# Performance work log

Measured on AMD Instinct MI355X. Metric: run time of the kernel, lower is better.

The kernel has to match this reference:

```python
import jax, jax.numpy as jnp
import numpy as np

N, E, IN_C, OUT_C, HEADS = 50000, 800000, 256, 256, 4
C = OUT_C // HEADS  # per-head channels = 64
BN_EPS = 1e-5


def setup_inputs() -> dict:
    key = jax.random.key(0)
    ks = jax.random.split(key, 16)
    inp = {
        'x': jax.random.normal(ks[0], (N, IN_C), dtype=jnp.float32),
        'edge_index': jax.random.randint(ks[1], (2, E), 0, N, dtype=jnp.int64),
        'edge_attr': jax.random.uniform(ks[2], (E, 1), dtype=jnp.float32),
        'spatial_coords': jax.random.normal(ks[3], (N, 2), dtype=jnp.float32),
        # GATConv params
        'W_gat': jax.random.normal(ks[4], (IN_C, HEADS * C), dtype=jnp.float32) * 0.05,
        'att_src': jax.random.normal(ks[5], (HEADS, C), dtype=jnp.float32) * 0.05,
        'att_dst': jax.random.normal(ks[6], (HEADS, C), dtype=jnp.float32) * 0.05,
        'bias_gat': jnp.zeros((HEADS * C,), dtype=jnp.float32),
        # spatial_attention MLP (computed but unused by the original forward)
        'w1': jax.random.normal(ks[7], (1, 64), dtype=jnp.float32) * 0.05,
        'b1': jnp.zeros((64,), dtype=jnp.float32),
        'w2': jax.random.normal(ks[8], (64, HEADS), dtype=jnp.float32) * 0.05,
        'b2': jnp.zeros((HEADS,), dtype=jnp.float32),
        # feature_transform: Linear + BatchNorm1d (eval stats) + ReLU (+Dropout=identity)
        'w_ft': jax.random.normal(ks[9], (IN_C, OUT_C), dtype=jnp.float32) * 0.05,
        'b_ft': jnp.zeros((OUT_C,), dtype=jnp.float32),
        'bn_gamma': jnp.ones((OUT_C,), dtype=jnp.float32),
        'bn_beta': jnp.zeros((OUT_C,), dtype=jnp.float32),
        'bn_mean': jax.random.normal(ks[10], (OUT_C,), dtype=jnp.float32) * 0.01,
        'bn_var': jax.random.uniform(ks[11], (OUT_C,), dtype=jnp.float32, minval=0.5, maxval=1.5),
    }
    return inp


def _forward(x, edge_index, edge_attr, W_gat, att_src, att_dst, bias_gat,
             w1, b1, w2, b2, w_ft, b_ft, bn_gamma, bn_beta, bn_mean, bn_var):
    n = x.shape[0]
    # add self-loops (PyG GATConv default)
    loop = jnp.arange(n, dtype=edge_index.dtype)
    src = jnp.concatenate([edge_index[0], loop])
    dst = jnp.concatenate([edge_index[1], loop])

    # linear transform: [N, heads, C]
    h = (x @ W_gat).reshape(n, HEADS, C)
    a_src = jnp.einsum('nhc,hc->nh', h, att_src)  # [N, H]
    a_dst = jnp.einsum('nhc,hc->nh', h, att_dst)  # [N, H]

    # per-edge attention logits, LeakyReLU(0.2)
    alpha = jax.nn.leaky_relu(a_src[src] + a_dst[dst], negative_slope=0.2)  # [Etot, H]
    # segment softmax over incoming edges of each destination node
    amax = jax.ops.segment_max(alpha, dst, num_segments=n)
    alpha = jnp.exp(alpha - amax[dst])
    denom = jax.ops.segment_sum(alpha, dst, num_segments=n)
    alpha = alpha / (denom[dst] + 1e-16)

    # weighted message aggregation
    msg = h[src] * alpha[:, :, None]                        # [Etot, H, C]
    agg = jax.ops.segment_sum(msg, dst, num_segments=n)     # [N, H, C]
    gat_out = agg.reshape(n, HEADS * C) + bias_gat

    # spatial attention weights (computed but UNUSED, matching original)
    spatial_weights = jax.nn.sigmoid(jax.nn.relu(edge_attr @ w1 + b1) @ w2 + b2)
    del spatial_weights

    # feature_transform (BatchNorm in eval mode, Dropout identity)
    y = x @ w_ft + b_ft
    y = (y - bn_mean) * jax.lax.rsqrt(bn_var + BN_EPS) * bn_gamma + bn_beta
    transformed = jax.nn.relu(y)

    return gat_out + transformed


def reference(x, edge_index, edge_attr, spatial_coords, W_gat, att_src, att_dst,
              bias_gat, w1, b1, w2, b2, w_ft, b_ft, bn_gamma, bn_beta, bn_mean, bn_var):
    # spatial_coords is accepted but unused by the original module's forward
    return _forward(x, edge_index, edge_attr, W_gat, att_src, att_dst, bias_gat,
                    w1, b1, w2, b2, w_ft, b_ft, bn_gamma, bn_beta, bn_mean, bn_var)
```

## Files before the change

### kernel.cpp

```cpp
#include <hip/hip_runtime.h>
#include <math.h>

typedef __attribute__((ext_vector_type(4))) float  f32x4;
typedef __attribute__((ext_vector_type(8))) short  short8;
typedef __attribute__((ext_vector_type(8))) unsigned short usx8;

__device__ __forceinline__ unsigned short f2bf(float f) {
    union { float f; unsigned int i; } c; c.f = f;
    unsigned int x = c.i;
    unsigned int r = (x + 0x7FFFu + ((x >> 16) & 1u)) >> 16;
    return (unsigned short)r;
}

__global__ __launch_bounds__(256) void k_prep1(
    int* __restrict__ zr, int zn,
    const float* __restrict__ Wg, const float* __restrict__ Wf,
    unsigned short* __restrict__ wbt, int nz) {
    int b = blockIdx.x;
    if (b < nz) {
        int i = b * 256 + threadIdx.x;
        if (i < zn) zr[i] = 0;
        return;
    }
    b -= nz;
    int idx = b * 256 + threadIdx.x;
    int c = idx >> 8;
    int k = idx & 255;
    float v = (c < 256) ? Wg[k * 256 + c] : Wf[k * 256 + (c - 256)];
    wbt[idx] = f2bf(v);
}

__global__ __launch_bounds__(256) void k_prep2(
    const float* __restrict__ x, unsigned short* __restrict__ xb, long total8, int nx,
    const int* __restrict__ ei, int* __restrict__ deg, int E) {
    int b = blockIdx.x;
    if (b < nx) {
        long i = (long)b * 256 + threadIdx.x;
        if (i >= total8) return;
        const f32x4* p = (const f32x4*)x;
        f32x4 v0 = p[2 * i], v1 = p[2 * i + 1];
        usx8 o;
        o[0] = f2bf(v0[0]); o[1] = f2bf(v0[1]); o[2] = f2bf(v0[2]); o[3] = f2bf(v0[3]);
        o[4] = f2bf(v1[0]); o[5] = f2bf(v1[1]); o[6] = f2bf(v1[2]); o[7] = f2bf(v1[3]);
        ((usx8*)xb)[i] = o;
        return;
    }
    int i = (b - nx) * 256 + threadIdx.x;
    if (i < E) atomicAdd(&deg[ei[E + i]], 1);
}

#define BM 128
#define BN 128

__global__ __launch_bounds__(256, 4) void k_gemm_scan(
    const unsigned short* __restrict__ xb,
    const unsigned short* __restrict__ wbt,
    unsigned short* __restrict__ hb,
    unsigned short* __restrict__ tb,
    float* __restrict__ out,
    const float* __restrict__ att_s, const float* __restrict__ att_d,
    float* __restrict__ a_src, float* __restrict__ a_dst,
    const float* __restrict__ b_ft, const float* __restrict__ bn_g,
    const float* __restrict__ bn_b, const float* __restrict__ bn_m,
    const float* __restrict__ bn_v, int M, int ngemm,
    const int* __restrict__ deg, int* __restrict__ offs, int* __restrict__ bsum) {
    __shared__ unsigned short As[128 * 64];
    __shared__ unsigned short Bs[128 * 64];
    __shared__ int tmp[256];

    if (blockIdx.x >= ngemm) {
        int b = blockIdx.x - ngemm, t = threadIdx.x;
        int base = b * 1024;
        int v[4];
#pragma unroll
        for (int j = 0; j < 4; j++) {
            int i = base + t * 4 + j;
            v[j] = (i < M) ? (deg[i] + 1) : 0;
        }
        int local = v[0] + v[1] + v[2] + v[3];
        tmp[t] = local;
        __syncthreads();
        for (int off = 1; off < 256; off <<= 1) {
            int xv = (t >= off) ? tmp[t - off] : 0;
            __syncthreads();
            tmp[t] += xv;
            __syncthreads();
        }
        int run = tmp[t] - local;
        if (t == 255) bsum[b] = tmp[255];
#pragma unroll
        for (int j = 0; j < 4; j++) {
            int i = base + t * 4 + j;
            if (i < M) offs[i] = run;
            run += v[j];
        }
        return;
    }

    const int t = threadIdx.x;
    const int w = t >> 6, l = t & 63;
    const int wr = w >> 1, wc = w & 1;
    const int bm0 = (blockIdx.x >> 2) * BM;
    const int bn0 = (blockIdx.x & 3) * BN;
    const int kg = l >> 4;
    const int lm = l & 15;

    const int srow = l >> 3;
    const int scol = ((l & 7) ^ srow) << 3;

    f32x4 acc[4][4] = {};

    for (int kk = 0; kk < 4; kk++) {
        const int k0 = kk * 64;
        __syncthreads();
#pragma unroll
        for (int j = 0; j < 4; j++) {
            int r = ((w * 4 + j) << 3) + srow;
            int ga = bm0 + r; if (ga >= M) ga = M - 1;
            __builtin_amdgcn_global_load_lds(
                (const __attribute__((address_space(1))) unsigned int*)
                    (xb + (long)ga * 256 + k0 + scol),
                (__attribute__((address_space(3))) unsigned int*)
                    (As + ((w * 4 + j) << 9)),
                16, 0, 0);
            __builtin_amdgcn_global_load_lds(
                (const __attribute__((address_space(1))) unsigned int*)
                    (wbt + (long)(bn0 + r) * 256 + k0 + scol),
                (__attribute__((address_space(3))) unsigned int*)
                    (Bs + ((w * 4 + j) << 9)),
                16, 0, 0);
        }
        __syncthreads();
#pragma unroll
        for (int ks = 0; ks < 2; ks++) {
            const int cb = (ks * 64 + kg * 16) ^ ((lm & 7) << 4);
            short8 afr[4], bfr[4];
#pragma unroll
            for (int mi = 0; mi < 4; mi++) {
                int row = wr * 64 + mi * 16 + lm;
                afr[mi] = *(const short8*)((const char*)As + row * 128 + cb);
            }
#pragma unroll
            for (int nj = 0; nj < 4; nj++) {
                int row = wc * 64 + nj * 16 + lm;
                bfr[nj] = *(const short8*)((const char*)Bs + row * 128 + cb);
            }
#pragma unroll
            for (int mi = 0; mi < 4; mi++)
#pragma unroll
                for (int nj = 0; nj < 4; nj++)
                    acc[mi][nj] = __builtin_amdgcn_mfma_f32_16x16x32_bf16(
                        afr[mi], bfr[nj], acc[mi][nj], 0, 0, 0);
        }
    }

    const bool isH = (bn0 < 256);
#pragma unroll
    for (int mi = 0; mi < 4; mi++) {
#pragma unroll
        for (int nj = 0; nj < 4; nj++) {
            int col = bn0 + wc * 64 + nj * 16 + lm;
            f32x4 a = acc[mi][nj];
            int rowbase = bm0 + wr * 64 + mi * 16 + kg * 4;
            if (isH) {
#pragma unroll
                for (int r = 0; r < 4; r++) {
                    int row = rowbase + r;
                    if (row < M) hb[(long)row * 256 + col] = f2bf(a[r]);
                }
            } else {
                int c2 = col - 256;
                float bft = b_ft[c2], mu = bn_m[c2];
                float iv = rsqrtf(bn_v[c2] + 1e-5f);
                float g = bn_g[c2], bt = bn_b[c2];
#pragma unroll
                for (int r = 0; r < 4; r++) {
                    int row = rowbase + r;
                    if (row < M) {
                        float v = (a[r] + bft - mu) * iv * g + bt;
                        v = v > 0.f ? v : 0.f;
                        if (tb) tb[(long)row * 256 + c2] = f2bf(v);
                        else    out[(long)row * 256 + c2] = v;
                    }
                }
            }
        }
    }

    if (isH) {
        const int head = (bn0 >> 6) + wc;
        float as_c[4], ad_c[4];
#pragma unroll
        for (int nj = 0; nj < 4; nj++) {
            as_c[nj] = att_s[head * 64 + nj * 16 + lm];
            ad_c[nj] = att_d[head * 64 + nj * 16 + lm];
        }
#pragma unroll
        for (int mi = 0; mi < 4; mi++) {
#pragma unroll
            for (int r = 0; r < 4; r++) {
                float s1 = 0.f, s2 = 0.f;
#pragma unroll
                for (int nj = 0; nj < 4; nj++) {
                    s1 = fmaf(acc[mi][nj][r], as_c[nj], s1);
                    s2 = fmaf(acc[mi][nj][r], ad_c[nj], s2);
                }
#pragma unroll
                for (int o = 1; o < 16; o <<= 1) {
                    s1 += __shfl_xor(s1, o);
                    s2 += __shfl_xor(s2, o);
                }
                int row = bm0 + wr * 64 + mi * 16 + kg * 4 + r;
                if (lm == 0 && row < M) {
                    a_src[(long)row * 4 + head] = s1;
                    a_dst[(long)row * 4 + head] = s2;
                }
            }
        }
    }
}

#define BK 32
__global__ __launch_bounds__(256) void k_gemm(
    const float* __restrict__ x, const unsigned short* __restrict__ wbt,
    unsigned short* __restrict__ hb, unsigned short* __restrict__ tb,
    float* __restrict__ out,
    const float* __restrict__ att_s, const float* __restrict__ att_d,
    float* __restrict__ a_src, float* __restrict__ a_dst,
    const float* __restrict__ b_ft, const float* __restrict__ bn_g,
    const float* __restrict__ bn_b, const float* __restrict__ bn_m,
    const float* __restrict__ bn_v, int M) {
    __shared__ unsigned short As[BM][BK + 8];
    __shared__ unsigned short Bs[BN][BK + 8];
    const int t = threadIdx.x;
    const int w = t >> 6, lane = t & 63;
    const int wr = w >> 1, wc = w & 1;
    const int bm0 = blockIdx.y * BM;
    const int bn0 = blockIdx.x * BN;
    const int kg = lane >> 4;
    const int lm = lane & 15;
    f32x4 acc[4][4] = {};
    for (int k0 = 0; k0 < 256; k0 += BK) {
        f32x4 a0[2], a1[2];
        usx8 bv[2];
#pragma unroll
        for (int s = 0; s < 2; s++) {
            int seg = t + s * 256;
            int row = seg >> 2;
            int off = (seg & 3) * 8;
            int grow = bm0 + row; if (grow >= M) grow = M - 1;
            const float* ap = x + (long)grow * 256 + k0 + off;
            a0[s] = *(const f32x4*)ap;
            a1[s] = *(const f32x4*)(ap + 4);
            bv[s] = *(const usx8*)(wbt + (long)(bn0 + row) * 256 + k0 + off);
        }
        __syncthreads();
#pragma unroll
        for (int s = 0; s < 2; s++) {
            int seg = t + s * 256;
            int row = seg >> 2;
            int off = (seg & 3) * 8;
            usx8 av;
            av[0] = f2bf(a0[s][0]); av[1] = f2bf(a0[s][1]);
            av[2] = f2bf(a0[s][2]); av[3] = f2bf(a0[s][3]);
            av[4] = f2bf(a1[s][0]); av[5] = f2bf(a1[s][1]);
            av[6] = f2bf(a1[s][2]); av[7] = f2bf(a1[s][3]);
            *(usx8*)&As[row][off] = av;
            *(usx8*)&Bs[row][off] = bv[s];
        }
        __syncthreads();
        short8 afr[4], bfr[4];
#pragma unroll
        for (int mi = 0; mi < 4; mi++)
            afr[mi] = *(const short8*)&As[wr * 64 + mi * 16 + lm][kg * 8];
#pragma unroll
        for (int nj = 0; nj < 4; nj++)
            bfr[nj] = *(const short8*)&Bs[wc * 64 + nj * 16 + lm][kg * 8];
#pragma unroll
        for (int mi = 0; mi < 4; mi++)
#pragma unroll
            for (int nj = 0; nj < 4; nj++)
                acc[mi][nj] = __builtin_amdgcn_mfma_f32_16x16x32_bf16(
                    afr[mi], bfr[nj], acc[mi][nj], 0, 0, 0);
        __syncthreads();
    }
    const bool isH = (bn0 < 256);
#pragma unroll
    for (int mi = 0; mi < 4; mi++) {
#pragma unroll
        for (int nj = 0; nj < 4; nj++) {
            int col = bn0 + wc * 64 + nj * 16 + lm;
            f32x4 a = acc[mi][nj];
            int rowbase = bm0 + wr * 64 + mi * 16 + kg * 4;
            if (isH) {
#pragma unroll
                for (int r = 0; r < 4; r++) {
                    int row = rowbase + r;
                    if (row < M) hb[(long)row * 256 + col] = f2bf(a[r]);
                }
            } else {
                int c2 = col - 256;
                float bft = b_ft[c2], mu = bn_m[c2];
                float iv = rsqrtf(bn_v[c2] + 1e-5f);
                float g = bn_g[c2], bt = bn_b[c2];
#pragma unroll
                for (int r = 0; r < 4; r++) {
                    int row = rowbase + r;
                    if (row < M) {
                        float v = (a[r] + bft - mu) * iv * g + bt;
                        v = v > 0.f ? v : 0.f;
                        if (tb) tb[(long)row * 256 + c2] = f2bf(v);
                        else    out[(long)row * 256 + c2] = v;
                    }
                }
            }
        }
    }
    if (isH) {
        const int head = (bn0 >> 6) + wc;
        float as_c[4], ad_c[4];
#pragma unroll
        for (int nj = 0; nj < 4; nj++) {
            as_c[nj] = att_s[head * 64 + nj * 16 + lm];
            ad_c[nj] = att_d[head * 64 + nj * 16 + lm];
        }
#pragma unroll
        for (int mi = 0; mi < 4; mi++) {
#pragma unroll
            for (int r = 0; r < 4; r++) {
                float s1 = 0.f, s2 = 0.f;
#pragma unroll
                for (int nj = 0; nj < 4; nj++) {
                    s1 = fmaf(acc[mi][nj][r], as_c[nj], s1);
                    s2 = fmaf(acc[mi][nj][r], ad_c[nj], s2);
                }
#pragma unroll
                for (int o = 1; o < 16; o <<= 1) {
                    s1 += __shfl_xor(s1, o);
                    s2 += __shfl_xor(s2, o);
                }
                int row = bm0 + wr * 64 + mi * 16 + kg * 4 + r;
                if (lm == 0 && row < M) {
                    a_src[(long)row * 4 + head] = s1;
                    a_dst[(long)row * 4 + head] = s2;
                }
            }
        }
    }
}

__global__ __launch_bounds__(256) void k_scan1(const int* __restrict__ deg,
                                               int* __restrict__ offs,
                                               int* __restrict__ bsum, int n) {
    __shared__ int tmp[256];
    int b = blockIdx.x, t = threadIdx.x;
    int base = b * 1024;
    int v[4];
#pragma unroll
    for (int j = 0; j < 4; j++) {
        int i = base + t * 4 + j;
        v[j] = (i < n) ? (deg[i] + 1) : 0;
    }
    int local = v[0] + v[1] + v[2] + v[3];
    tmp[t] = local;
    __syncthreads();
    for (int off = 1; off < 256; off <<= 1) {
        int xv = (t >= off) ? tmp[t - off] : 0;
        __syncthreads();
        tmp[t] += xv;
        __syncthreads();
    }
    int run = tmp[t] - local;
    if (t == 255) bsum[b] = tmp[255];
#pragma unroll
    for (int j = 0; j < 4; j++) {
        int i = base + t * 4 + j;
        if (i < n) offs[i] = run;
        run += v[j];
    }
}

__global__ void k_scan3f(int* __restrict__ offs, const int* __restrict__ bsum,
                         int* __restrict__ srcs, int n) {
    int i = blockIdx.x * blockDim.x + threadIdx.x;
    if (i >= n) return;
    int nbi = i >> 10;
    int s = 0;
    for (int j = 0; j < nbi; j++) s += bsum[j];
    int o = offs[i] + s;
    offs[i] = o;
    srcs[o] = i;
}
__global__ void k_scatter(const int* __restrict__ ei, const int* __restrict__ offs,
                          int* __restrict__ cursor, int* __restrict__ srcs, int E) {
    int i = blockIdx.x * blockDim.x + threadIdx.x;
    if (i >= E) return;
    int d = ei[E + i];
    int pos = atomicAdd(&cursor[d], 1);
    srcs[offs[d] + 1 + pos] = ei[i];
}

__global__ __launch_bounds__(256, 4) void k_agg(
    const int* __restrict__ offs, const int* __restrict__ srcs,
    const unsigned short* __restrict__ hb,
    const float* __restrict__ a_src, const float* __restrict__ a_dst,
    const float* __restrict__ bias_gat, const unsigned short* __restrict__ tb,
    float* __restrict__ out, int N, int E) {
    const int n = (blockIdx.x * 256 + threadIdx.x) >> 6;
    const int l = threadIdx.x & 63;
    if (n >= N) return;
    const int head = l >> 4;
    const int sub = l & 15;
    const int beg = offs[n];
    const int end = (n + 1 < N) ? offs[n + 1] : (E + N);
    const uint2* hp = (const uint2*)hb + l;

    const float ad = a_dst[(long)n * 4 + head];
    f32x4 acc = {};
    float den = 0.f;

    for (int base = beg; base < end; base += 16) {
        const int len = min(16, end - base);
        int sv = 0;
        float wsel = 0.f;
        if (base + sub < end) {
            sv = srcs[base + sub];
            float lv = a_src[(long)sv * 4 + head] + ad;
            lv = fmaxf(lv, 0.2f * lv);
            wsel = __expf(lv);
        }

        if (len == 16) {
            uint2 hv[16];
#pragma unroll
            for (int i = 0; i < 16; ++i) {
                int src = __shfl(sv, i);
                const uint2* ap = hp + ((long)src << 6);
                asm volatile("global_load_dwordx2 %0, %1, off"
                             : "=v"(hv[i]) : "v"(ap));
            }
            float wg[16];
#pragma unroll
            for (int i = 0; i < 16; ++i) wg[i] = __shfl(wsel, (l & 48) + i);
            asm volatile("s_waitcnt vmcnt(0)" ::: "memory");
            __builtin_amdgcn_sched_barrier(0);
#pragma unroll
            for (int i = 0; i < 16; ++i) {
                den += wg[i];
                acc[0] = fmaf(wg[i], __uint_as_float(hv[i].x << 16), acc[0]);
                acc[1] = fmaf(wg[i], __uint_as_float(hv[i].x & 0xFFFF0000u), acc[1]);
                acc[2] = fmaf(wg[i], __uint_as_float(hv[i].y << 16), acc[2]);
                acc[3] = fmaf(wg[i], __uint_as_float(hv[i].y & 0xFFFF0000u), acc[3]);
            }
        } else {
            for (int i = 0; i < len; ++i) {
                int src = __shfl(sv, i);
                float wgt = __shfl(wsel, (l & 48) + i);
                uint2 hv = hp[(long)src << 6];
                den += wgt;
                acc[0] = fmaf(wgt, __uint_as_float(hv.x << 16), acc[0]);
                acc[1] = fmaf(wgt, __uint_as_float(hv.x & 0xFFFF0000u), acc[1]);
                acc[2] = fmaf(wgt, __uint_as_float(hv.y << 16), acc[2]);
                acc[3] = fmaf(wgt, __uint_as_float(hv.y & 0xFFFF0000u), acc[3]);
            }
        }
    }

    const float inv = 1.f / (den + 1e-16f);
    const float4 bv = ((const float4*)bias_gat)[l];
    float4 trf;
    const long rowoff = ((long)n << 8) + l * 4;
    if (tb) {
        uint2 tv = ((const uint2*)(tb + ((long)n << 8)))[l];
        trf.x = __uint_as_float(tv.x << 16);
        trf.y = __uint_as_float(tv.x & 0xFFFF0000u);
        trf.z = __uint_as_float(tv.y << 16);
        trf.w = __uint_as_float(tv.y & 0xFFFF0000u);
    } else {
        trf = *(const float4*)(out + rowoff);
    }
    float4 r;
    r.x = acc[0] * inv + bv.x + trf.x;
    r.y = acc[1] * inv + bv.y + trf.y;
    r.z = acc[2] * inv + bv.z + trf.z;
    r.w = acc[3] * inv + bv.w + trf.w;
    *(float4*)(out + rowoff) = r;
}

extern "C" void kernel_launch(void* const* d_in, const int* in_sizes, int n_in,
                              void* d_out, int out_size, void* d_ws, size_t ws_size,
                              hipStream_t stream) {
    const float* x        = (const float*)d_in[0];
    const int*   ei       = (const int*)d_in[1];
    const float* W_gat    = (const float*)d_in[4];
    const float* att_src  = (const float*)d_in[5];
    const float* att_dst  = (const float*)d_in[6];
    const float* bias_gat = (const float*)d_in[7];
    const float* w_ft     = (const float*)d_in[12];
    const float* b_ft     = (const float*)d_in[13];
    const float* bn_g     = (const float*)d_in[14];
    const float* bn_b     = (const float*)d_in[15];
    const float* bn_m     = (const float*)d_in[16];
    const float* bn_v     = (const float*)d_in[17];
    float* out = (float*)d_out;

    const int N = in_sizes[0] / 256;
    const int E = in_sizes[1] / 2;
    const int ETOT = E + N;

    char* p = (char*)d_ws;
    char* pend = p + ws_size;
    auto alloc = [&](size_t bytes) {
        void* r = (void*)p;
        p += (bytes + 255) & ~(size_t)255;
        return r;
    };
    unsigned short* wbt  = (unsigned short*)alloc((size_t)512 * 256 * 2);
    unsigned short* hb   = (unsigned short*)alloc((size_t)N * 256 * 2);
    float* a_src = (float*)alloc((size_t)N * 4 * 4);
    float* a_dst = (float*)alloc((size_t)N * 4 * 4);
    char* z0 = p;
    int* deg    = (int*)alloc((size_t)N * 4);
    int* cursor = (int*)alloc((size_t)N * 4);
    char* z1 = p;
    int* offs   = (int*)alloc((size_t)(N + 1) * 4);
    int* bsum   = (int*)alloc((size_t)256 * 4);
    int* srcs   = (int*)alloc((size_t)ETOT * 4);
    unsigned short* xb = (unsigned short*)alloc((size_t)N * 256 * 2);
    if (p > pend) xb = nullptr;
    unsigned short* tb = (unsigned short*)alloc((size_t)N * 256 * 2);
    if (p > pend) tb = nullptr;

    const int zn = (int)((z1 - z0) / 4);
    const int nz = (zn + 255) / 256;
    const long total8 = (long)N * 256 / 8;
    const int nx = xb ? (int)((total8 + 255) / 256) : 0;
    const int ce = (E + 255) / 256;
    const int nb = (N + 1023) / 1024;
    const int ngemm = 4 * ((N + BM - 1) / BM);

    k_prep1<<<nz + 512, 256, 0, stream>>>((int*)z0, zn, W_gat, w_ft, wbt, nz);

    if (xb) {
        k_prep2<<<nx + ce, 256, 0, stream>>>(x, xb, total8, nx, ei, deg, E);
        k_gemm_scan<<<ngemm + nb, 256, 0, stream>>>(
            xb, wbt, hb, tb, out, att_src, att_dst, a_src, a_dst,
            b_ft, bn_g, bn_b, bn_m, bn_v, N, ngemm, deg, offs, bsum);
    } else {
        k_prep2<<<ce, 256, 0, stream>>>(x, nullptr, 0, 0, ei, deg, E);
        dim3 gg(4, (N + BM - 1) / BM);
        k_gemm<<<gg, 256, 0, stream>>>(x, wbt, hb, tb, out, att_src, att_dst,
                                       a_src, a_dst, b_ft, bn_g, bn_b, bn_m, bn_v, N);
        k_scan1<<<nb, 256, 0, stream>>>(deg, offs, bsum, N);
    }

    k_scan3f<<<(N + 255) / 256, 256, 0, stream>>>(offs, bsum, srcs, N);
    k_scatter<<<ce, 256, 0, stream>>>(ei, offs, cursor, srcs, E);

    k_agg<<<(N * 64 + 255) / 256, 256, 0, stream>>>(offs, srcs, hb, a_src, a_dst,
                                                    bias_gat, tb, out, N, E);
}
```

Measured before the change: 220.2 us.

## Double-buffer GEMM LDS tiles with K=32 stages to overlap loads and MFMA

The GEMM K loop changes from four 64-wide stages in a single LDS buffer to eight 32-wide stages with two ping-pong buffers. The next tile is prefetched via global_load_lds while MFMAs run on the current one, so global-to-LDS latency is meant to hide behind compute. Total LDS use stays the same. In exchange it adds more barriers, uses a new XOR swizzle for the narrower rows, and waits on vmcnt(0) each iteration, which may limit how much overlap actually happens.

```diff
diff --git a/kernel.cpp b/kernel.cpp
--- a/kernel.cpp
+++ b/kernel.cpp
@@ -64,8 +64,8 @@
     const float* __restrict__ bn_b, const float* __restrict__ bn_m,
     const float* __restrict__ bn_v, int M, int ngemm,
     const int* __restrict__ deg, int* __restrict__ offs, int* __restrict__ bsum) {
-    __shared__ unsigned short As[128 * 64];
-    __shared__ unsigned short Bs[128 * 64];
+    __shared__ unsigned short As[2][128 * 32];
+    __shared__ unsigned short Bs[2][128 * 32];
     __shared__ int tmp[256];
 
     if (blockIdx.x >= ngemm) {
@@ -105,53 +105,65 @@
     const int kg = l >> 4;
     const int lm = l & 15;
 
-    const int srow = l >> 3;
-    const int scol = ((l & 7) ^ srow) << 3;
-
-    f32x4 acc[4][4] = {};
-
-    for (int kk = 0; kk < 4; kk++) {
-        const int k0 = kk * 64;
-        __syncthreads();
-#pragma unroll
-        for (int j = 0; j < 4; j++) {
-            int r = ((w * 4 + j) << 3) + srow;
-            int ga = bm0 + r; if (ga >= M) ga = M - 1;
+    int rowA[2], colA[2];
+#pragma unroll
+    for (int j = 0; j < 2; j++) {
+        int s = t + j * 256;
+        int row = s >> 2;
+        rowA[j] = row;
+        colA[j] = (((s & 3) ^ (row & 3)) << 3);
+    }
+
+    auto issue = [&](int kkv) {
+        const int k0_ = kkv * 32;
+        const int bsel = kkv & 1;
+#pragma unroll
+        for (int j = 0; j < 2; j++) {
+            int s = t + j * 256;
+            int row = rowA[j];
+            int ga = bm0 + row; if (ga >= M) ga = M - 1;
             __builtin_amdgcn_global_load_lds(
                 (const __attribute__((address_space(1))) unsigned int*)
-                    (xb + (long)ga * 256 + k0 + scol),
+                    (xb + (long)ga * 256 + k0_ + colA[j]),
                 (__attribute__((address_space(3))) unsigned int*)
-                    (As + ((w * 4 + j) << 9)),
+                    (&As[bsel][s << 3]),
                 16, 0, 0);
             __builtin_amdgcn_global_load_lds(
                 (const __attribute__((address_space(1))) unsigned int*)
-                    (wbt + (long)(bn0 + r) * 256 + k0 + scol),
+                    (wbt + (long)(bn0 + row) * 256 + k0_ + colA[j]),
                 (__attribute__((address_space(3))) unsigned int*)
-                    (Bs + ((w * 4 + j) << 9)),
+                    (&Bs[bsel][s << 3]),
                 16, 0, 0);
         }
-        __syncthreads();
-#pragma unroll
-        for (int ks = 0; ks < 2; ks++) {
-            const int cb = (ks * 64 + kg * 16) ^ ((lm & 7) << 4);
-            short8 afr[4], bfr[4];
-#pragma unroll
-            for (int mi = 0; mi < 4; mi++) {
-                int row = wr * 64 + mi * 16 + lm;
-                afr[mi] = *(const short8*)((const char*)As + row * 128 + cb);
-            }
-#pragma unroll
-            for (int nj = 0; nj < 4; nj++) {
-                int row = wc * 64 + nj * 16 + lm;
-                bfr[nj] = *(const short8*)((const char*)Bs + row * 128 + cb);
-            }
-#pragma unroll
-            for (int mi = 0; mi < 4; mi++)
-#pragma unroll
-                for (int nj = 0; nj < 4; nj++)
-                    acc[mi][nj] = __builtin_amdgcn_mfma_f32_16x16x32_bf16(
-                        afr[mi], bfr[nj], acc[mi][nj], 0, 0, 0);
-        }
+    };
+
+    f32x4 acc[4][4] = {};
+    const int cb = ((kg ^ (lm & 3)) << 4);
+
+    issue(0);
+    for (int kk = 0; kk < 8; kk++) {
+        const int cur = kk & 1;
+        asm volatile("s_waitcnt vmcnt(0)" ::: "memory");
+        __builtin_amdgcn_s_barrier();
+        __builtin_amdgcn_sched_barrier(0);
+        if (kk < 7) issue(kk + 1);
+        short8 afr[4], bfr[4];
+#pragma unroll
+        for (int mi = 0; mi < 4; mi++) {
+            int row = wr * 64 + mi * 16 + lm;
+            afr[mi] = *(const short8*)((const char*)&As[cur][0] + row * 64 + cb);
+        }
+#pragma unroll
+        for (int nj = 0; nj < 4; nj++) {
+            int row = wc * 64 + nj * 16 + lm;
+            bfr[nj] = *(const short8*)((const char*)&Bs[cur][0] + row * 64 + cb);
+        }
+#pragma unroll
+        for (int mi = 0; mi < 4; mi++)
+#pragma unroll
+            for (int nj = 0; nj < 4; nj++)
+                acc[mi][nj] = __builtin_amdgcn_mfma_f32_16x16x32_bf16(
+                    afr[mi], bfr[nj], acc[mi][nj], 0, 0, 0);
     }
 
     const bool isH = (bn0 < 256);
```

After: 226.3 us. +2.8%, slower.
